# Kernel optimization log

Measured on AMD Instinct MI355X. Metric: run time of the kernel, lower is better.

## Reference

```python
import jax, jax.numpy as jnp
import numpy as np

B, Tin, Tout = 256, 32, 29
Venc, Vdec = 29, 72
E = 256; H = 256; L = 3; G = 4 * H; D = 2 * L  # bidirectional dirs * layers


def lstm_step(x, h, c, Wih0, Wih1, Whh, b):
    """One timestep of a 3-layer bidirectional LSTM (torch gate order i,f,g,o).
    x: [B, in], h/c: [D, B, H] in torch layout (layer-major, dir-minor)."""
    new_h, new_c = [], []
    inp = x
    for l in range(L):
        outs = []
        for d in range(2):
            idx = 2 * l + d
            Wih = Wih0[d] if l == 0 else Wih1[l - 1, d]
            g = inp @ Wih.T + h[idx] @ Whh[l, d].T + b[l, d]
            i_g, f_g, g_g, o_g = jnp.split(g, 4, axis=-1)
            cc = jax.nn.sigmoid(f_g) * c[idx] + jax.nn.sigmoid(i_g) * jnp.tanh(g_g)
            hh = jax.nn.sigmoid(o_g) * jnp.tanh(cc)
            new_h.append(hh); new_c.append(cc); outs.append(hh)
        inp = jnp.concatenate(outs, axis=-1)  # feeds next layer: [B, 2H]
    return jnp.stack(new_h), jnp.stack(new_c), inp


def proj(hid, W1, b1, W2, b2):
    """Linear over hidden dim then Linear over the layer*dir dim -- the exact
    math of torch's linear1 -> permute(2,1,0) -> linear2 -> permute(2,1,0)."""
    hn = jnp.einsum('lbh,gh->lbg', hid, W1) + b1            # [D, B, H]
    return jnp.einsum('lbh,ml->mbh', hn, W2) + b2[:, None, None]


def setup_inputs() -> dict:
    key = jax.random.key(0)
    ks = iter(jax.random.split(key, 64))
    def p(shape, scale=0.06):
        return jax.random.normal(next(ks), shape, jnp.float32) * scale
    return {
        "input": jax.random.randint(next(ks), (B, Tin), 0, Venc),
        "target": jax.random.randint(next(ks), (B, Tout), 0, Vdec),
        "teacher_force": 1,
        "enc_emb": p((Venc, E)), "dec_emb": p((Vdec, E)),
        "enc_Wih0": p((2, G, E)), "enc_Wih1": p((L - 1, 2, G, 2 * H)),
        "enc_Whh": p((L, 2, G, H)), "enc_b": p((L, 2, G)),
        "dec_Wih0": p((2, G, E)), "dec_Wih1": p((L - 1, 2, G, 2 * H)),
        "dec_Whh": p((L, 2, G, H)), "dec_b": p((L, 2, G)),
        "lin_h_W1": p((H, H)), "lin_h_b1": p((H,)), "lin_h_W2": p((D, D)), "lin_h_b2": p((D,)),
        "lin_c_W1": p((H, H)), "lin_c_b1": p((H,)), "lin_c_W2": p((D, D)), "lin_c_b2": p((D,)),
        "lin_a_W1": p((H, H)), "lin_a_b1": p((H,)), "lin_a_W2": p((D, D)), "lin_a_b2": p((D,)),
        "attn_W": p((E, E + H)), "attn_b": p((E,)),
        "fc_W": p((Vdec, 2 * H)), "fc_b": p((Vdec,)),
    }


def reference(input, target, teacher_force, enc_emb, dec_emb, enc_Wih0, enc_Wih1, enc_Whh, enc_b, dec_Wih0, dec_Wih1, dec_Whh, dec_b, lin_h_W1, lin_h_b1, lin_h_W2, lin_h_b2, lin_c_W1, lin_c_b1, lin_c_W2, lin_c_b2, lin_a_W1, lin_a_b1, lin_a_W2, lin_a_b2, attn_W, attn_b, fc_W, fc_b):
    Bb = input.shape[0]
    h0 = jnp.zeros((D, Bb, H), jnp.float32)

    # ---- encoder: step LSTM over Tin, projecting hidden per step for attention ----
    def enc_step(carry, x_t):
        h, c = carry
        h, c, _ = lstm_step(enc_emb[x_t], h, c, enc_Wih0, enc_Wih1, enc_Whh, enc_b)
        return (h, c), proj(h, lin_a_W1, lin_a_b1, lin_a_W2, lin_a_b2)

    (h, c), encoder_outputs = jax.lax.scan(enc_step, (h0, h0), input.T)  # [Tin, D, B, H]

    # ---- encoder->decoder state bridging (linear over H, linear over D) ----
    dec_h = proj(h, lin_h_W1, lin_h_b1, lin_h_W2, lin_h_b2)
    dec_c = proj(c, lin_c_W1, lin_c_b1, lin_c_W2, lin_c_b2)

    def dec_core(h, c, tok):
        emb = dec_emb[tok]                                # [B, E]
        energies = h[None] * encoder_outputs              # [Tin, D, B, H]
        aw = jax.nn.softmax(energies, axis=0)             # attn over source time
        ctx = (aw * encoder_outputs).sum(0).mean(0)       # [B, H]
        x = jnp.concatenate([emb, ctx], -1) @ attn_W.T + attn_b
        h, c, top = lstm_step(x, h, c, dec_Wih0, dec_Wih1, dec_Whh, dec_b)
        return h, c, top @ fc_W.T + fc_b, aw.sum(-1)      # logits [B,V], aw [Tin,D,B]

    if teacher_force:
        def step(carry, tok):
            h, c = carry
            h, c, logits, _ = dec_core(h, c, tok)
            return (h, c), logits
        _, logits_seq = jax.lax.scan(step, (dec_h, dec_c), target[:, :Tout - 1].T)
        attn_seq = jnp.zeros((Tout - 1, Tin, D, Bb), jnp.float32)
    else:
        def step(carry, _):
            h, c, tok = carry
            h, c, logits, aw = dec_core(h, c, tok)
            nxt = jnp.argmax(jax.nn.softmax(logits, -1), -1).astype(tok.dtype)
            return (h, c, nxt), (logits, aw)
        tok0 = jnp.ones((Bb,), input.dtype)
        _, (logits_seq, attn_seq) = jax.lax.scan(step, (dec_h, dec_c, tok0), None, length=Tout - 1)

    pred0 = jnp.zeros((1, Bb, Vdec), jnp.float32).at[0, :, 1].set(1.0)
    predicted = jnp.concatenate([pred0, logits_seq], 0)   # [Tout, B, Vdec]
    attn_weights = jnp.concatenate([jnp.zeros((1, Tin, D, Bb), jnp.float32), attn_seq], 0)
    return predicted, attn_weights
```

## Files before the change

### kernel.cpp

```cpp
#include <hip/hip_runtime.h>
#include <math.h>

#define BB 256
#define TIN 32
#define TOUT 29
#define VDEC 72
#define EDIM 256
#define HDIM 256
#define DD 6
#define BH (BB*HDIM)

typedef unsigned short u16;
typedef unsigned int u32;
typedef __bf16 bf16x8 __attribute__((ext_vector_type(8)));
typedef float f32x4 __attribute__((ext_vector_type(4)));
typedef u16 u16x8 __attribute__((ext_vector_type(8)));

__device__ __forceinline__ float sigmf(float x){ return 1.0f/(1.0f+expf(-x)); }
__device__ __forceinline__ u16 f2bf(float f){
  u32 u = __builtin_bit_cast(u32, f);
  u32 r = (u + 0x7fffu + ((u>>16)&1u)) >> 16;
  return (u16)r;
}
__device__ __forceinline__ float bf2f(u16 s){
  u32 u = ((u32)s)<<16; return __builtin_bit_cast(float, u);
}
__device__ __forceinline__ bf16x8 ldbf8(const u16* p){
  u16x8 t = *(const u16x8*)p; return __builtin_bit_cast(bf16x8, t);
}
__device__ __forceinline__ f32x4 mfma16(bf16x8 a, bf16x8 b, f32x4 c){
  return __builtin_amdgcn_mfma_f32_16x16x32_bf16(a, b, c, 0, 0, 0);
}

__global__ void fill_zero_u32(u32* __restrict__ p, int n){
  int i = blockIdx.x*256 + threadIdx.x;
  if (i < n) p[i] = 0u;
}

__global__ void init_out_kernel(float* __restrict__ out, int n){
  int i = blockIdx.x*256 + threadIdx.x;
  if (i >= n) return;
  float v = 0.0f;
  if (i < BB*VDEC && (i % VDEC) == 1) v = 1.0f;
  out[i] = v;
}

__global__ void bias2d_kernel(const float* __restrict__ W2a, const float* __restrict__ b1a, const float* __restrict__ b2a,
                              const float* __restrict__ W2h, const float* __restrict__ b1h, const float* __restrict__ b2h,
                              const float* __restrict__ W2c, const float* __restrict__ b1c, const float* __restrict__ b2c,
                              float* __restrict__ outp){
  int g = threadIdx.x;
  const float* W2[3] = {W2a, W2h, W2c};
  const float* b1[3] = {b1a, b1h, b1c};
  const float* b2[3] = {b2a, b2h, b2c};
  for (int p = 0; p < 3; p++)
    for (int m = 0; m < 6; m++){
      float s = 0.f;
      for (int l = 0; l < 6; l++) s += W2[p][m*6+l];
      outp[p*1536 + m*256 + g] = s * b1[p][g] + b2[p][m];
    }
}

__global__ void embed_enc_kernel(const int* __restrict__ input, const float* __restrict__ enc_emb,
                                 u16* __restrict__ x_emb){
  int i = blockIdx.x*256 + threadIdx.x;
  int e = i & 255, b = (i >> 8) & 255, t = i >> 16;
  x_emb[i] = f2bf(enc_emb[(size_t)input[b*TIN + t]*EDIM + e]);
}

__global__ void pack_w_kernel(const float* __restrict__ Wih, const float* __restrict__ Whh,
                              u16* __restrict__ dst, int K1, int K, int permute){
  int k = blockIdx.x*256 + threadIdx.x;
  int row = blockIdx.y;
  int d = row >> 10, rr = row & 1023;
  int g;
  if (permute){
    int ht = rr >> 6, r = rr & 63;
    g = (r>>4)*256 + ht*16 + (r&15);
  } else g = rr;
  float v;
  if (k < K1) v = Wih[((size_t)d*1024 + g)*K1 + k];
  else        v = Whh[((size_t)d*1024 + g)*256 + (k - K1)];
  dst[(size_t)row*K + k] = f2bf(v);
}

__global__ void mix_kernel(const float* __restrict__ inp, float* __restrict__ outp,
                           const float* __restrict__ W2, int n){
  int i = blockIdx.x*256 + threadIdx.x;
  if (i >= n) return;
  int h = i & 255, b = (i >> 8) & 255, t = i >> 16;
  size_t base = ((size_t)t*6)*BH + (size_t)b*256 + h;
  float v[6];
  #pragma unroll
  for (int l = 0; l < 6; l++) v[l] = inp[base + (size_t)l*BH];
  #pragma unroll
  for (int m = 0; m < 6; m++){
    float s = 0.f;
    #pragma unroll
    for (int l = 0; l < 6; l++) s += W2[m*6+l]*v[l];
    outp[base + (size_t)m*BH] = s;
  }
}

__global__ __launch_bounds__(256) void gemmN256_kernel(const float* __restrict__ A, float* __restrict__ C,
                                                       const float* __restrict__ W,
                                                       const float* __restrict__ bias2d,
                                                       u16* __restrict__ Cbf){
  __shared__ float As[32][33];
  __shared__ float Ws[256][34];
  int tid = threadIdx.x;
  int m_base = blockIdx.x * 32;
  int rg = tid >> 5, cg = tid & 31;
  float acc[4][8];
  #pragma unroll
  for (int i=0;i<4;i++)
    #pragma unroll
    for (int j=0;j<8;j++) acc[i][j]=0.f;
  for (int k0 = 0; k0 < 256; k0 += 32){
    #pragma unroll
    for (int p=0;p<4;p++) As[rg + p*8][cg] = A[(size_t)(m_base + rg + p*8)*256 + k0 + cg];
    #pragma unroll
    for (int p=0;p<32;p++) Ws[rg + p*8][cg] = W[(size_t)(rg + p*8)*256 + k0 + cg];
    __syncthreads();
    #pragma unroll
    for (int kk=0; kk<32; kk++){
      float a[4], w[8];
      #pragma unroll
      for (int i=0;i<4;i++) a[i] = As[rg*4+i][kk];
      #pragma unroll
      for (int j=0;j<8;j++) w[j] = Ws[cg*8+j][kk];
      #pragma unroll
      for (int i=0;i<4;i++)
        #pragma unroll
        for (int j=0;j<8;j++) acc[i][j] += a[i]*w[j];
    }
    __syncthreads();
  }
  #pragma unroll
  for (int i=0;i<4;i++){
    int row = m_base + rg*4 + i;
    int bm = (row >> 8) % 6;
    #pragma unroll
    for (int j=0;j<8;j++){
      float v = acc[i][j] + bias2d[bm*256 + cg*8 + j];
      C[(size_t)row*256 + cg*8 + j] = v;
      if (Cbf) Cbf[(size_t)row*256 + cg*8 + j] = f2bf(v);
    }
  }
}

__global__ __launch_bounds__(256) void lstm_stage_mfma(
    const u16* __restrict__ inp, int lda, int K1,
    const u16* __restrict__ Wpk,
    const float* __restrict__ bias_l,
    const u16* __restrict__ hR, u16* __restrict__ hW,
    float* __restrict__ cBuf, u16* __restrict__ inp_out,
    float* __restrict__ h_all_t, int l){
  __shared__ __align__(16) u16 As[32][72];
  __shared__ __align__(16) u16 Ws[64][72];
  __shared__ float Gt[4][32][17];
  int tid = threadIdx.x;
  int m_base = blockIdx.x*32;
  int d = blockIdx.y >> 4, ht = blockIdx.y & 15;
  int idx = 2*l + d;
  int K = K1 + 256;
  const u16* Wblk = Wpk + (size_t)((d*16+ht)*64)*K;
  const u16* A2 = hR + (size_t)idx*BH;
  int q = tid >> 6, lane = tid & 63;
  int ar = tid >> 3, kp = (tid & 7)*8;
  f32x4 acc0 = {0.f,0.f,0.f,0.f}, acc1 = {0.f,0.f,0.f,0.f};
  for (int c0 = 0; c0 < K; c0 += 64){
    int col = c0 + kp;
    const u16* ap = (col < K1) ? inp + (size_t)(m_base+ar)*lda + col
                               : A2  + (size_t)(m_base+ar)*HDIM + (col - K1);
    uint4 av  = *(const uint4*)ap;
    uint4 wv0 = *(const uint4*)(Wblk + (size_t)ar*K + col);
    uint4 wv1 = *(const uint4*)(Wblk + (size_t)(ar+32)*K + col);
    __syncthreads();
    *(uint4*)&As[ar][kp] = av;
    *(uint4*)&Ws[ar][kp] = wv0;
    *(uint4*)&Ws[ar+32][kp] = wv1;
    __syncthreads();
    #pragma unroll
    for (int kh = 0; kh < 2; kh++){
      int kb = kh*32 + (lane>>4)*8;
      bf16x8 a0 = ldbf8(&As[lane & 15][kb]);
      bf16x8 a1 = ldbf8(&As[16 + (lane & 15)][kb]);
      bf16x8 bq = ldbf8(&Ws[q*16 + (lane & 15)][kb]);
      acc0 = mfma16(a0, bq, acc0);
      acc1 = mfma16(a1, bq, acc1);
    }
  }
  int hh = lane & 15, rq = lane >> 4;
  #pragma unroll
  for (int r = 0; r < 4; r++){
    Gt[q][rq*4 + r][hh]      = acc0[r];
    Gt[q][16 + rq*4 + r][hh] = acc1[r];
  }
  __syncthreads();
  const float* bias = bias_l + d*1024;
  #pragma unroll
  for (int it = 0; it < 2; it++){
    int id = tid + it*256;
    int bb = id >> 4, h2 = id & 15;
    int b = m_base + bb, h = ht*16 + h2;
    float iv = Gt[0][bb][h2] + bias[h];
    float fv = Gt[1][bb][h2] + bias[256 + h];
    float gv = Gt[2][bb][h2] + bias[512 + h];
    float ov = Gt[3][bb][h2] + bias[768 + h];
    size_t off = (size_t)idx*BH + (size_t)b*HDIM + h;
    float cold = cBuf[off];
    float cc = sigmf(fv)*cold + sigmf(iv)*tanhf(gv);
    float hv = sigmf(ov)*tanhf(cc);
    cBuf[off] = cc;
    u16 hb = f2bf(hv);
    hW[off] = hb;
    inp_out[(size_t)b*512 + d*HDIM + h] = hb;
    if (h_all_t) h_all_t[off] = hv;
  }
}

__global__ __launch_bounds__(256) void xw_mfma(
    const u16* __restrict__ emb, const u16* __restrict__ ctx,
    const u16* __restrict__ Wpk, const float* __restrict__ bias,
    u16* __restrict__ xw){
  __shared__ __align__(16) u16 As[32][72];
  __shared__ __align__(16) u16 Ws[64][72];
  int tid = threadIdx.x;
  int m_base = blockIdx.x*32;
  int n_base = blockIdx.y*64;
  int q = tid >> 6, lane = tid & 63;
  int ar = tid >> 3, kp = (tid & 7)*8;
  const u16* Wblk = Wpk + (size_t)n_base*512;
  f32x4 acc0 = {0.f,0.f,0.f,0.f}, acc1 = {0.f,0.f,0.f,0.f};
  for (int c0 = 0; c0 < 512; c0 += 64){
    int col = c0 + kp;
    const u16* ap = (col < 256) ? emb + (size_t)(m_base+ar)*256 + col
                                : ctx + (size_t)(m_base+ar)*256 + (col - 256);
    uint4 av  = *(const uint4*)ap;
    uint4 wv0 = *(const uint4*)(Wblk + (size_t)ar*512 + col);
    uint4 wv1 = *(const uint4*)(Wblk + (size_t)(ar+32)*512 + col);
    __syncthreads();
    *(uint4*)&As[ar][kp] = av;
    *(uint4*)&Ws[ar][kp] = wv0;
    *(uint4*)&Ws[ar+32][kp] = wv1;
    __syncthreads();
    #pragma unroll
    for (int kh = 0; kh < 2; kh++){
      int kb = kh*32 + (lane>>4)*8;
      bf16x8 a0 = ldbf8(&As[lane & 15][kb]);
      bf16x8 a1 = ldbf8(&As[16 + (lane & 15)][kb]);
      bf16x8 bq = ldbf8(&Ws[q*16 + (lane & 15)][kb]);
      acc0 = mfma16(a0, bq, acc0);
      acc1 = mfma16(a1, bq, acc1);
    }
  }
  int hh = lane & 15, rq = lane >> 4;
  int n = n_base + q*16 + hh;
  float bv = bias[n];
  #pragma unroll
  for (int r = 0; r < 4; r++){
    xw[(size_t)(m_base + rq*4 + r)*256 + n]      = f2bf(acc0[r] + bv);
    xw[(size_t)(m_base + 16 + rq*4 + r)*256 + n] = f2bf(acc1[r] + bv);
  }
}

__global__ void attn_tok_kernel(const u16* __restrict__ hR, const float* __restrict__ eo,
                                u16* __restrict__ ctx, const int* __restrict__ tf,
                                float* __restrict__ attn_out, int step,
                                const int* __restrict__ target, const float* __restrict__ pred,
                                const float* __restrict__ dec_emb, u16* __restrict__ emb){
  int blk = blockIdx.x, tid = threadIdx.x;
  if (blk < 256){
    int i = blk*256 + tid;
    int hc = i & 255, b = i >> 8;
    bool wa = (tf[0] == 0);
    float acc = 0.f;
    for (int d = 0; d < DD; d++){
      float hv = bf2f(hR[(size_t)d*BH + (size_t)b*256 + hc]);
      const float* ep = eo + (size_t)d*BH + (size_t)b*256 + hc;
      float se = 0.f, ac = 0.f;
      for (int t = 0; t < TIN; t++){
        float ev = ep[(size_t)t*(DD*BH)];
        float e = expf(hv*ev);
        se += e; ac += e*ev;
      }
      acc += ac/se;
      if (wa){
        float inv = 1.f/se;
        for (int t = 0; t < TIN; t++){
          float ev = ep[(size_t)t*(DD*BH)];
          atomicAdd(&attn_out[(((size_t)(step+1)*TIN + t)*DD + d)*BB + b], expf(hv*ev)*inv);
        }
      }
    }
    ctx[i] = f2bf(acc*(1.0f/6.0f));
  } else {
    int j = (blk - 256)*256 + tid;
    int b = j >> 6, e4 = (j & 63)*4;
    int tok;
    if (tf[0]) tok = target[b*TOUT + step];
    else if (step == 0) tok = 1;
    else {
      const float* lg = pred + ((size_t)step*BB + b)*VDEC;
      tok = 0; float bv = lg[0];
      for (int v = 1; v < VDEC; v++){ float x = lg[v]; if (x > bv){ bv = x; tok = v; } }
    }
    #pragma unroll
    for (int r = 0; r < 4; r++)
      emb[(size_t)b*EDIM + e4 + r] = f2bf(dec_emb[(size_t)tok*EDIM + e4 + r]);
  }
}

__global__ void fc_kernel(const u16* __restrict__ top, const float* __restrict__ fc_W,
                          const float* __restrict__ fc_b, float* __restrict__ outp, int step){
  __shared__ float s[512];
  int b = blockIdx.x, tid = threadIdx.x;
  s[tid]       = bf2f(top[(size_t)b*512 + tid]);
  s[tid + 256] = bf2f(top[(size_t)b*512 + 256 + tid]);
  __syncthreads();
  if (tid < VDEC){
    float a = fc_b[tid];
    for (int k = 0; k < 512; k++) a += s[k]*fc_W[(size_t)tid*512 + k];
    outp[((size_t)(step+1)*BB + b)*VDEC + tid] = a;
  }
}


extern "C" void kernel_launch(void* const* d_in, const int* in_sizes, int n_in,
                              void* d_out, int out_size, void* d_ws, size_t ws_size,
                              hipStream_t stream){
  (void)in_sizes; (void)n_in; (void)out_size; (void)ws_size;
  const int*   input    = (const int*)d_in[0];
  const int*   target   = (const int*)d_in[1];
  const int*   tf       = (const int*)d_in[2];
  const float* enc_emb  = (const float*)d_in[3];
  const float* dec_emb  = (const float*)d_in[4];
  const float* enc_Wih0 = (const float*)d_in[5];
  const float* enc_Wih1 = (const float*)d_in[6];
  const float* enc_Whh  = (const float*)d_in[7];
  const float* enc_b    = (const float*)d_in[8];
  const float* dec_Wih0 = (const float*)d_in[9];
  const float* dec_Wih1 = (const float*)d_in[10];
  const float* dec_Whh  = (const float*)d_in[11];
  const float* dec_b    = (const float*)d_in[12];
  const float* lin_h_W1 = (const float*)d_in[13];
  const float* lin_h_b1 = (const float*)d_in[14];
  const float* lin_h_W2 = (const float*)d_in[15];
  const float* lin_h_b2 = (const float*)d_in[16];
  const float* lin_c_W1 = (const float*)d_in[17];
  const float* lin_c_b1 = (const float*)d_in[18];
  const float* lin_c_W2 = (const float*)d_in[19];
  const float* lin_c_b2 = (const float*)d_in[20];
  const float* lin_a_W1 = (const float*)d_in[21];
  const float* lin_a_b1 = (const float*)d_in[22];
  const float* lin_a_W2 = (const float*)d_in[23];
  const float* lin_a_b2 = (const float*)d_in[24];
  const float* attn_W   = (const float*)d_in[25];
  const float* attn_b   = (const float*)d_in[26];
  const float* fc_W     = (const float*)d_in[27];
  const float* fc_b     = (const float*)d_in[28];
  float* out = (float*)d_out;

  char* base = (char*)d_ws;
  size_t off = 0;
  auto alloc = [&](size_t bytes)->char*{
    char* p = base + off; off += (bytes + 255) & ~(size_t)255; return p;
  };
  float* h_all  = (float*)alloc(sizeof(float)*(size_t)TIN*DD*BH);
  float* tmp6   = (float*)alloc(sizeof(float)*(size_t)DD*BH);
  float* dec_c  = (float*)alloc(sizeof(float)*(size_t)DD*BH);
  float* bias2d = (float*)alloc(sizeof(float)*3*6*256);
  u16*   enc_hA = (u16*)alloc(sizeof(u16)*(size_t)DD*BH + sizeof(float)*(size_t)DD*BH);
  float* enc_c  = (float*)(enc_hA + (size_t)DD*BH);
  u16* enc_hB = (u16*)alloc(sizeof(u16)*(size_t)DD*BH);
  u16* dec_hA = (u16*)alloc(sizeof(u16)*(size_t)DD*BH);
  u16* dec_hB = (u16*)alloc(sizeof(u16)*(size_t)DD*BH);
  u16* x_emb  = (u16*)alloc(sizeof(u16)*(size_t)TIN*BB*EDIM);
  u16* bufA   = (u16*)alloc(sizeof(u16)*(size_t)BB*512);
  u16* bufB   = (u16*)alloc(sizeof(u16)*(size_t)BB*512);
  u16* emb    = (u16*)alloc(sizeof(u16)*(size_t)BB*256);
  u16* ctxb   = (u16*)alloc(sizeof(u16)*(size_t)BB*256);
  u16* xw     = (u16*)alloc(sizeof(u16)*(size_t)BB*256);
  u16* wp_e0  = (u16*)alloc(sizeof(u16)*(size_t)2048*512);
  u16* wp_e1  = (u16*)alloc(sizeof(u16)*(size_t)2048*768);
  u16* wp_e2  = (u16*)alloc(sizeof(u16)*(size_t)2048*768);
  u16* wp_d0  = (u16*)alloc(sizeof(u16)*(size_t)2048*512);
  u16* wp_d1  = (u16*)alloc(sizeof(u16)*(size_t)2048*768);
  u16* wp_d2  = (u16*)alloc(sizeof(u16)*(size_t)2048*768);
  u16* wp_at  = (u16*)alloc(sizeof(u16)*(size_t)256*512);

  const int outn = TOUT*BB*VDEC + TOUT*TIN*DD*BB;
  init_out_kernel<<<(outn+255)/256, 256, 0, stream>>>(out, outn);
  fill_zero_u32<<<(DD*BH*6/4 + 255)/256, 256, 0, stream>>>((u32*)enc_hA, DD*BH*6/4);
  bias2d_kernel<<<1, 256, 0, stream>>>(lin_a_W2, lin_a_b1, lin_a_b2,
                                       lin_h_W2, lin_h_b1, lin_h_b2,
                                       lin_c_W2, lin_c_b1, lin_c_b2, bias2d);
  embed_enc_kernel<<<(TIN*BB*EDIM)/256, 256, 0, stream>>>(input, enc_emb, x_emb);
  pack_w_kernel<<<dim3(2,2048), 256, 0, stream>>>(enc_Wih0, enc_Whh,                       wp_e0, 256, 512, 1);
  pack_w_kernel<<<dim3(3,2048), 256, 0, stream>>>(enc_Wih1, enc_Whh + 2*1024*256,          wp_e1, 512, 768, 1);
  pack_w_kernel<<<dim3(3,2048), 256, 0, stream>>>(enc_Wih1 + (size_t)2*1024*512, enc_Whh + 4*1024*256, wp_e2, 512, 768, 1);
  pack_w_kernel<<<dim3(2,2048), 256, 0, stream>>>(dec_Wih0, dec_Whh,                       wp_d0, 256, 512, 1);
  pack_w_kernel<<<dim3(3,2048), 256, 0, stream>>>(dec_Wih1, dec_Whh + 2*1024*256,          wp_d1, 512, 768, 1);
  pack_w_kernel<<<dim3(3,2048), 256, 0, stream>>>(dec_Wih1 + (size_t)2*1024*512, dec_Whh + 4*1024*256, wp_d2, 512, 768, 1);
  pack_w_kernel<<<dim3(2,256),  256, 0, stream>>>(attn_W, attn_W ,               wp_at, 512, 512, 0);

  dim3 sgrid(8, 32);
  for (int t = 0; t < TIN; t++){
    const u16* hRb = (t & 1) ? enc_hB : enc_hA;
    u16*       hWb = (t & 1) ? enc_hA : enc_hB;
    float* hat = h_all + (size_t)t*DD*BH;
    lstm_stage_mfma<<<sgrid,256,0,stream>>>(x_emb + (size_t)t*BB*EDIM, 256, 256, wp_e0,
        enc_b,        hRb, hWb, enc_c, bufA, hat, 0);
    lstm_stage_mfma<<<sgrid,256,0,stream>>>(bufA, 512, 512, wp_e1,
        enc_b + 2048, hRb, hWb, enc_c, bufB, hat, 1);
    lstm_stage_mfma<<<sgrid,256,0,stream>>>(bufB, 512, 512, wp_e2,
        enc_b + 4096, hRb, hWb, enc_c, bufA, hat, 2);
  }
  mix_kernel<<<BH/256, 256, 0, stream>>>(h_all + (size_t)31*DD*BH, tmp6, lin_h_W2, BH);
  gemmN256_kernel<<<(DD*BB)/32, 256, 0, stream>>>(tmp6, tmp6, lin_h_W1, bias2d + 1536, dec_hA);
  mix_kernel<<<BH/256, 256, 0, stream>>>(enc_c, tmp6, lin_c_W2, BH);
  gemmN256_kernel<<<(DD*BB)/32, 256, 0, stream>>>(tmp6, dec_c, lin_c_W1, bias2d + 3072, nullptr);
  mix_kernel<<<(TIN*BH)/256, 256, 0, stream>>>(h_all, h_all, lin_a_W2, TIN*BH);
  gemmN256_kernel<<<(TIN*DD*BB)/32, 256, 0, stream>>>(h_all, h_all, lin_a_W1, bias2d, nullptr);

  float* attn_out = out + (size_t)TOUT*BB*VDEC;
  for (int i = 0; i < TOUT-1; i++){
    const u16* hRb = (i & 1) ? dec_hB : dec_hA;
    u16*       hWb = (i & 1) ? dec_hA : dec_hB;
    attn_tok_kernel<<<320, 256, 0, stream>>>(hRb, h_all, ctxb, tf, attn_out, i,
                                             target, out, dec_emb, emb);
    xw_mfma<<<dim3(8,4), 256, 0, stream>>>(emb, ctxb, wp_at, attn_b, xw);
    lstm_stage_mfma<<<sgrid,256,0,stream>>>(xw, 256, 256, wp_d0,
        dec_b,        hRb, hWb, dec_c, bufA, nullptr, 0);
    lstm_stage_mfma<<<sgrid,256,0,stream>>>(bufA, 512, 512, wp_d1,
        dec_b + 2048, hRb, hWb, dec_c, bufB, nullptr, 1);
    lstm_stage_mfma<<<sgrid,256,0,stream>>>(bufB, 512, 512, wp_d2,
        dec_b + 4096, hRb, hWb, dec_c, bufA, nullptr, 2);
    fc_kernel<<<BB, 256, 0, stream>>>(bufA, fc_W, fc_b, out, i);
  }
}
```

Baseline: 3.429 ms.

## Fold attention linear into decoder weights, fuse fc into attention, double-buffer LSTM loads

Precomputes Wih0·attn_W and the matching bias so the decoder's attention-combine GEMM disappears and layer 0 reads the concatenated [emb, ctx] directly. The fc projection and argmax move into the attention/token kernel for the next step, which drops one launch per decoder step. Encoder outputs are now stored in bf16, halving attention read traffic. The LSTM stage kernel is templated on K, uses double-buffered register and shared-memory prefetch with a single barrier per iteration, and switches to fast exp/tanh. This trades accuracy (bf16 encoder outputs, folded weights rounded to bf16, approximate transcendentals) for fewer launches and less memory traffic.

```diff
diff --git a/kernel.cpp b/kernel.cpp
--- a/kernel.cpp
+++ b/kernel.cpp
@@ -16,7 +16,8 @@
 typedef float f32x4 __attribute__((ext_vector_type(4)));
 typedef u16 u16x8 __attribute__((ext_vector_type(8)));
 
-__device__ __forceinline__ float sigmf(float x){ return 1.0f/(1.0f+expf(-x)); }
+__device__ __forceinline__ float sigmf(float x){ return 1.0f/(1.0f+__expf(-x)); }
+__device__ __forceinline__ float tanhf_fast(float x){ return 1.0f - 2.0f/(1.0f+__expf(2.0f*x)); }
 __device__ __forceinline__ u16 f2bf(float f){
   u32 u = __builtin_bit_cast(u32, f);
   u32 r = (u + 0x7fffu + ((u>>16)&1u)) >> 16;
@@ -69,19 +70,46 @@
 }
 
 __global__ void pack_w_kernel(const float* __restrict__ Wih, const float* __restrict__ Whh,
-                              u16* __restrict__ dst, int K1, int K, int permute){
+                              u16* __restrict__ dst, int K1, int K){
   int k = blockIdx.x*256 + threadIdx.x;
   int row = blockIdx.y;
   int d = row >> 10, rr = row & 1023;
-  int g;
-  if (permute){
-    int ht = rr >> 6, r = rr & 63;
-    g = (r>>4)*256 + ht*16 + (r&15);
-  } else g = rr;
+  int ht = rr >> 6, r = rr & 63;
+  int g = (r>>4)*256 + ht*16 + (r&15);
   float v;
   if (k < K1) v = Wih[((size_t)d*1024 + g)*K1 + k];
   else        v = Whh[((size_t)d*1024 + g)*256 + (k - K1)];
   dst[(size_t)row*K + k] = f2bf(v);
+}
+
+__global__ void pack_wfused_kernel(const float* __restrict__ Wih0, const float* __restrict__ attn_W,
+                                   const float* __restrict__ Whh, u16* __restrict__ dst){
+  int k = blockIdx.x*256 + threadIdx.x;
+  int row = blockIdx.y;
+  int d = row >> 10, rr = row & 1023;
+  int ht = rr >> 6, r = rr & 63;
+  int g = (r>>4)*256 + ht*16 + (r&15);
+  float v;
+  if (k >= 512) v = Whh[((size_t)d*1024 + g)*256 + (k - 512)];
+  else {
+    const float* wr = Wih0 + ((size_t)d*1024 + g)*256;
+    float s = 0.f;
+    #pragma unroll 4
+    for (int o = 0; o < 256; o++) s += wr[o] * attn_W[(size_t)o*512 + k];
+    v = s;
+  }
+  dst[(size_t)row*768 + k] = f2bf(v);
+}
+
+__global__ void biasfold_kernel(const float* __restrict__ Wih0, const float* __restrict__ attn_b,
+                                const float* __restrict__ dec_b, float* __restrict__ outb){
+  int i = blockIdx.x*256 + threadIdx.x;
+  int d = i >> 10, g = i & 1023;
+  const float* wr = Wih0 + ((size_t)d*1024 + g)*256;
+  float s = dec_b[d*1024 + g];
+  #pragma unroll 4
+  for (int o = 0; o < 256; o++) s += wr[o]*attn_b[o];
+  outb[i] = s;
 }
 
 __global__ void mix_kernel(const float* __restrict__ inp, float* __restrict__ outp,
@@ -143,50 +171,66 @@
     #pragma unroll
     for (int j=0;j<8;j++){
       float v = acc[i][j] + bias2d[bm*256 + cg*8 + j];
-      C[(size_t)row*256 + cg*8 + j] = v;
+      if (C)   C[(size_t)row*256 + cg*8 + j] = v;
       if (Cbf) Cbf[(size_t)row*256 + cg*8 + j] = f2bf(v);
     }
   }
 }
 
+template<int K1>
 __global__ __launch_bounds__(256) void lstm_stage_mfma(
-    const u16* __restrict__ inp, int lda, int K1,
+    const u16* __restrict__ inp,
     const u16* __restrict__ Wpk,
     const float* __restrict__ bias_l,
     const u16* __restrict__ hR, u16* __restrict__ hW,
     float* __restrict__ cBuf, u16* __restrict__ inp_out,
     float* __restrict__ h_all_t, int l){
-  __shared__ __align__(16) u16 As[32][72];
-  __shared__ __align__(16) u16 Ws[64][72];
+  constexpr int K = K1 + 256;
+  constexpr int NIT = K >> 6;
+  __shared__ __align__(16) u16 As[2][32][72];
+  __shared__ __align__(16) u16 Ws[2][64][72];
   __shared__ float Gt[4][32][17];
   int tid = threadIdx.x;
   int m_base = blockIdx.x*32;
   int d = blockIdx.y >> 4, ht = blockIdx.y & 15;
   int idx = 2*l + d;
-  int K = K1 + 256;
   const u16* Wblk = Wpk + (size_t)((d*16+ht)*64)*K;
-  const u16* A2 = hR + (size_t)idx*BH;
   int q = tid >> 6, lane = tid & 63;
   int ar = tid >> 3, kp = (tid & 7)*8;
+  const u16* aRow  = inp + (size_t)(m_base+ar)*K1 + kp;
+  const u16* hRow  = hR + (size_t)idx*BH + (size_t)(m_base+ar)*HDIM + kp - K1;
+  const u16* wRow0 = Wblk + (size_t)ar*K + kp;
+  const u16* wRow1 = Wblk + (size_t)(ar+32)*K + kp;
+  uint4 aP[2], w0P[2], w1P[2];
+  #pragma unroll
+  for (int pf = 0; pf < 2; pf++){
+    int c0 = pf*64;
+    const u16* ap = (c0 + kp < K1) ? aRow : hRow;
+    aP[pf]  = *(const uint4*)(ap + c0);
+    w0P[pf] = *(const uint4*)(wRow0 + c0);
+    w1P[pf] = *(const uint4*)(wRow1 + c0);
+  }
   f32x4 acc0 = {0.f,0.f,0.f,0.f}, acc1 = {0.f,0.f,0.f,0.f};
-  for (int c0 = 0; c0 < K; c0 += 64){
-    int col = c0 + kp;
-    const u16* ap = (col < K1) ? inp + (size_t)(m_base+ar)*lda + col
-                               : A2  + (size_t)(m_base+ar)*HDIM + (col - K1);
-    uint4 av  = *(const uint4*)ap;
-    uint4 wv0 = *(const uint4*)(Wblk + (size_t)ar*K + col);
-    uint4 wv1 = *(const uint4*)(Wblk + (size_t)(ar+32)*K + col);
-    __syncthreads();
-    *(uint4*)&As[ar][kp] = av;
-    *(uint4*)&Ws[ar][kp] = wv0;
-    *(uint4*)&Ws[ar+32][kp] = wv1;
+  #pragma unroll
+  for (int i = 0; i < NIT; i++){
+    int p = i & 1;
+    *(uint4*)&As[p][ar][kp]     = aP[p];
+    *(uint4*)&Ws[p][ar][kp]     = w0P[p];
+    *(uint4*)&Ws[p][ar+32][kp]  = w1P[p];
+    int c0n = (i+2) << 6;
+    if (c0n < K){
+      const u16* ap = (c0n + kp < K1) ? aRow : hRow;
+      aP[p]  = *(const uint4*)(ap + c0n);
+      w0P[p] = *(const uint4*)(wRow0 + c0n);
+      w1P[p] = *(const uint4*)(wRow1 + c0n);
+    }
     __syncthreads();
     #pragma unroll
     for (int kh = 0; kh < 2; kh++){
       int kb = kh*32 + (lane>>4)*8;
-      bf16x8 a0 = ldbf8(&As[lane & 15][kb]);
-      bf16x8 a1 = ldbf8(&As[16 + (lane & 15)][kb]);
-      bf16x8 bq = ldbf8(&Ws[q*16 + (lane & 15)][kb]);
+      bf16x8 a0 = ldbf8(&As[p][lane & 15][kb]);
+      bf16x8 a1 = ldbf8(&As[p][16 + (lane & 15)][kb]);
+      bf16x8 bq = ldbf8(&Ws[p][q*16 + (lane & 15)][kb]);
       acc0 = mfma16(a0, bq, acc0);
       acc1 = mfma16(a1, bq, acc1);
     }
@@ -210,8 +254,8 @@
     float ov = Gt[3][bb][h2] + bias[768 + h];
     size_t off = (size_t)idx*BH + (size_t)b*HDIM + h;
     float cold = cBuf[off];
-    float cc = sigmf(fv)*cold + sigmf(iv)*tanhf(gv);
-    float hv = sigmf(ov)*tanhf(cc);
+    float cc = sigmf(fv)*cold + sigmf(iv)*tanhf_fast(gv);
+    float hv = sigmf(ov)*tanhf_fast(cc);
     cBuf[off] = cc;
     u16 hb = f2bf(hv);
     hW[off] = hb;
@@ -220,95 +264,68 @@
   }
 }
 
-__global__ __launch_bounds__(256) void xw_mfma(
-    const u16* __restrict__ emb, const u16* __restrict__ ctx,
-    const u16* __restrict__ Wpk, const float* __restrict__ bias,
-    u16* __restrict__ xw){
-  __shared__ __align__(16) u16 As[32][72];
-  __shared__ __align__(16) u16 Ws[64][72];
-  int tid = threadIdx.x;
-  int m_base = blockIdx.x*32;
-  int n_base = blockIdx.y*64;
-  int q = tid >> 6, lane = tid & 63;
-  int ar = tid >> 3, kp = (tid & 7)*8;
-  const u16* Wblk = Wpk + (size_t)n_base*512;
-  f32x4 acc0 = {0.f,0.f,0.f,0.f}, acc1 = {0.f,0.f,0.f,0.f};
-  for (int c0 = 0; c0 < 512; c0 += 64){
-    int col = c0 + kp;
-    const u16* ap = (col < 256) ? emb + (size_t)(m_base+ar)*256 + col
-                                : ctx + (size_t)(m_base+ar)*256 + (col - 256);
-    uint4 av  = *(const uint4*)ap;
-    uint4 wv0 = *(const uint4*)(Wblk + (size_t)ar*512 + col);
-    uint4 wv1 = *(const uint4*)(Wblk + (size_t)(ar+32)*512 + col);
-    __syncthreads();
-    *(uint4*)&As[ar][kp] = av;
-    *(uint4*)&Ws[ar][kp] = wv0;
-    *(uint4*)&Ws[ar+32][kp] = wv1;
-    __syncthreads();
-    #pragma unroll
-    for (int kh = 0; kh < 2; kh++){
-      int kb = kh*32 + (lane>>4)*8;
-      bf16x8 a0 = ldbf8(&As[lane & 15][kb]);
-      bf16x8 a1 = ldbf8(&As[16 + (lane & 15)][kb]);
-      bf16x8 bq = ldbf8(&Ws[q*16 + (lane & 15)][kb]);
-      acc0 = mfma16(a0, bq, acc0);
-      acc1 = mfma16(a1, bq, acc1);
-    }
-  }
-  int hh = lane & 15, rq = lane >> 4;
-  int n = n_base + q*16 + hh;
-  float bv = bias[n];
-  #pragma unroll
-  for (int r = 0; r < 4; r++){
-    xw[(size_t)(m_base + rq*4 + r)*256 + n]      = f2bf(acc0[r] + bv);
-    xw[(size_t)(m_base + 16 + rq*4 + r)*256 + n] = f2bf(acc1[r] + bv);
-  }
-}
-
-__global__ void attn_tok_kernel(const u16* __restrict__ hR, const float* __restrict__ eo,
-                                u16* __restrict__ ctx, const int* __restrict__ tf,
+__global__ void attn_tok_kernel(const u16* __restrict__ hR, const u16* __restrict__ eo,
+                                u16* __restrict__ cat, const int* __restrict__ tf,
                                 float* __restrict__ attn_out, int step,
-                                const int* __restrict__ target, const float* __restrict__ pred,
-                                const float* __restrict__ dec_emb, u16* __restrict__ emb){
+                                const int* __restrict__ target, float* __restrict__ outp,
+                                const float* __restrict__ dec_emb, const u16* __restrict__ top,
+                                const float* __restrict__ fc_W, const float* __restrict__ fc_b){
   int blk = blockIdx.x, tid = threadIdx.x;
+  __shared__ float s[512];
+  __shared__ float lg[VDEC];
+  __shared__ int tokS;
   if (blk < 256){
-    int i = blk*256 + tid;
-    int hc = i & 255, b = i >> 8;
+    int b = blk, hc = tid;
     bool wa = (tf[0] == 0);
     float acc = 0.f;
     for (int d = 0; d < DD; d++){
       float hv = bf2f(hR[(size_t)d*BH + (size_t)b*256 + hc]);
-      const float* ep = eo + (size_t)d*BH + (size_t)b*256 + hc;
+      const u16* ep = eo + (size_t)d*BH + (size_t)b*256 + hc;
       float se = 0.f, ac = 0.f;
+      #pragma unroll 8
       for (int t = 0; t < TIN; t++){
-        float ev = ep[(size_t)t*(DD*BH)];
-        float e = expf(hv*ev);
+        float ev = bf2f(ep[(size_t)t*(DD*BH)]);
+        float e = __expf(hv*ev);
         se += e; ac += e*ev;
       }
       acc += ac/se;
       if (wa){
         float inv = 1.f/se;
         for (int t = 0; t < TIN; t++){
-          float ev = ep[(size_t)t*(DD*BH)];
-          atomicAdd(&attn_out[(((size_t)(step+1)*TIN + t)*DD + d)*BB + b], expf(hv*ev)*inv);
+          float ev = bf2f(ep[(size_t)t*(DD*BH)]);
+          atomicAdd(&attn_out[(((size_t)(step+1)*TIN + t)*DD + d)*BB + b], __expf(hv*ev)*inv);
         }
       }
     }
-    ctx[i] = f2bf(acc*(1.0f/6.0f));
+    cat[(size_t)b*512 + 256 + hc] = f2bf(acc*(1.0f/6.0f));
   } else {
-    int j = (blk - 256)*256 + tid;
-    int b = j >> 6, e4 = (j & 63)*4;
+    int b = blk - 256;
+    if (step > 0){
+      s[tid]       = bf2f(top[(size_t)b*512 + tid]);
+      s[tid + 256] = bf2f(top[(size_t)b*512 + 256 + tid]);
+      __syncthreads();
+      if (tid < VDEC){
+        float a = fc_b[tid];
+        #pragma unroll 4
+        for (int k = 0; k < 512; k++) a += s[k]*fc_W[(size_t)tid*512 + k];
+        outp[((size_t)step*BB + b)*VDEC + tid] = a;
+        lg[tid] = a;
+      }
+      __syncthreads();
+    }
     int tok;
     if (tf[0]) tok = target[b*TOUT + step];
     else if (step == 0) tok = 1;
     else {
-      const float* lg = pred + ((size_t)step*BB + b)*VDEC;
-      tok = 0; float bv = lg[0];
-      for (int v = 1; v < VDEC; v++){ float x = lg[v]; if (x > bv){ bv = x; tok = v; } }
-    }
-    #pragma unroll
-    for (int r = 0; r < 4; r++)
-      emb[(size_t)b*EDIM + e4 + r] = f2bf(dec_emb[(size_t)tok*EDIM + e4 + r]);
+      if (tid == 0){
+        int bi = 0; float bv = lg[0];
+        for (int v = 1; v < VDEC; v++){ float x = lg[v]; if (x > bv){ bv = x; bi = v; } }
+        tokS = bi;
+      }
+      __syncthreads();
+      tok = tokS;
+    }
+    cat[(size_t)b*512 + tid] = f2bf(dec_emb[(size_t)tok*EDIM + tid]);
   }
 }
 
@@ -321,6 +338,7 @@
   __syncthreads();
   if (tid < VDEC){
     float a = fc_b[tid];
+    #pragma unroll 4
     for (int k = 0; k < 512; k++) a += s[k]*fc_W[(size_t)tid*512 + k];
     outp[((size_t)(step+1)*BB + b)*VDEC + tid] = a;
   }
@@ -379,16 +397,15 @@
   u16* x_emb  = (u16*)alloc(sizeof(u16)*(size_t)TIN*BB*EDIM);
   u16* bufA   = (u16*)alloc(sizeof(u16)*(size_t)BB*512);
   u16* bufB   = (u16*)alloc(sizeof(u16)*(size_t)BB*512);
-  u16* emb    = (u16*)alloc(sizeof(u16)*(size_t)BB*256);
-  u16* ctxb   = (u16*)alloc(sizeof(u16)*(size_t)BB*256);
-  u16* xw     = (u16*)alloc(sizeof(u16)*(size_t)BB*256);
+  u16* cat    = (u16*)alloc(sizeof(u16)*(size_t)BB*512);
+  u16* eo_bf  = (u16*)alloc(sizeof(u16)*(size_t)TIN*DD*BH);
   u16* wp_e0  = (u16*)alloc(sizeof(u16)*(size_t)2048*512);
   u16* wp_e1  = (u16*)alloc(sizeof(u16)*(size_t)2048*768);
   u16* wp_e2  = (u16*)alloc(sizeof(u16)*(size_t)2048*768);
-  u16* wp_d0  = (u16*)alloc(sizeof(u16)*(size_t)2048*512);
+  u16* wp_d0f = (u16*)alloc(sizeof(u16)*(size_t)2048*768);
   u16* wp_d1  = (u16*)alloc(sizeof(u16)*(size_t)2048*768);
   u16* wp_d2  = (u16*)alloc(sizeof(u16)*(size_t)2048*768);
-  u16* wp_at  = (u16*)alloc(sizeof(u16)*(size_t)256*512);
+  float* fb0  = (float*)alloc(sizeof(float)*2048);
 
   const int outn = TOUT*BB*VDEC + TOUT*TIN*DD*BB;
   init_out_kernel<<<(outn+255)/256, 256, 0, stream>>>(out, outn);
@@ -397,46 +414,45 @@
                                        lin_h_W2, lin_h_b1, lin_h_b2,
                                        lin_c_W2, lin_c_b1, lin_c_b2, bias2d);
   embed_enc_kernel<<<(TIN*BB*EDIM)/256, 256, 0, stream>>>(input, enc_emb, x_emb);
-  pack_w_kernel<<<dim3(2,2048), 256, 0, stream>>>(enc_Wih0, enc_Whh,                       wp_e0, 256, 512, 1);
-  pack_w_kernel<<<dim3(3,2048), 256, 0, stream>>>(enc_Wih1, enc_Whh + 2*1024*256,          wp_e1, 512, 768, 1);
-  pack_w_kernel<<<dim3(3,2048), 256, 0, stream>>>(enc_Wih1 + (size_t)2*1024*512, enc_Whh + 4*1024*256, wp_e2, 512, 768, 1);
-  pack_w_kernel<<<dim3(2,2048), 256, 0, stream>>>(dec_Wih0, dec_Whh,                       wp_d0, 256, 512, 1);
-  pack_w_kernel<<<dim3(3,2048), 256, 0, stream>>>(dec_Wih1, dec_Whh + 2*1024*256,          wp_d1, 512, 768, 1);
-  pack_w_kernel<<<dim3(3,2048), 256, 0, stream>>>(dec_Wih1 + (size_t)2*1024*512, dec_Whh + 4*1024*256, wp_d2, 512, 768, 1);
-  pack_w_kernel<<<dim3(2,256),  256, 0, stream>>>(attn_W, attn_W ,               wp_at, 512, 512, 0);
+  pack_w_kernel<<<dim3(2,2048), 256, 0, stream>>>(enc_Wih0, enc_Whh,                       wp_e0, 256, 512);
+  pack_w_kernel<<<dim3(3,2048), 256, 0, stream>>>(enc_Wih1, enc_Whh + 2*1024*256,          wp_e1, 512, 768);
+  pack_w_kernel<<<dim3(3,2048), 256, 0, stream>>>(enc_Wih1 + (size_t)2*1024*512, enc_Whh + 4*1024*256, wp_e2, 512, 768);
+  pack_wfused_kernel<<<dim3(3,2048), 256, 0, stream>>>(dec_Wih0, attn_W, dec_Whh,          wp_d0f);
+  biasfold_kernel<<<8, 256, 0, stream>>>(dec_Wih0, attn_b, dec_b, fb0);
+  pack_w_kernel<<<dim3(3,2048), 256, 0, stream>>>(dec_Wih1, dec_Whh + 2*1024*256,          wp_d1, 512, 768);
+  pack_w_kernel<<<dim3(3,2048), 256, 0, stream>>>(dec_Wih1 + (size_t)2*1024*512, dec_Whh + 4*1024*256, wp_d2, 512, 768);
 
   dim3 sgrid(8, 32);
   for (int t = 0; t < TIN; t++){
     const u16* hRb = (t & 1) ? enc_hB : enc_hA;
     u16*       hWb = (t & 1) ? enc_hA : enc_hB;
     float* hat = h_all + (size_t)t*DD*BH;
-    lstm_stage_mfma<<<sgrid,256,0,stream>>>(x_emb + (size_t)t*BB*EDIM, 256, 256, wp_e0,
+    lstm_stage_mfma<256><<<sgrid,256,0,stream>>>(x_emb + (size_t)t*BB*EDIM, wp_e0,
         enc_b,        hRb, hWb, enc_c, bufA, hat, 0);
-    lstm_stage_mfma<<<sgrid,256,0,stream>>>(bufA, 512, 512, wp_e1,
+    lstm_stage_mfma<512><<<sgrid,256,0,stream>>>(bufA, wp_e1,
         enc_b + 2048, hRb, hWb, enc_c, bufB, hat, 1);
-    lstm_stage_mfma<<<sgrid,256,0,stream>>>(bufB, 512, 512, wp_e2,
+    lstm_stage_mfma<512><<<sgrid,256,0,stream>>>(bufB, wp_e2,
         enc_b + 4096, hRb, hWb, enc_c, bufA, hat, 2);
   }
   mix_kernel<<<BH/256, 256, 0, stream>>>(h_all + (size_t)31*DD*BH, tmp6, lin_h_W2, BH);
-  gemmN256_kernel<<<(DD*BB)/32, 256, 0, stream>>>(tmp6, tmp6, lin_h_W1, bias2d + 1536, dec_hA);
+  gemmN256_kernel<<<(DD*BB)/32, 256, 0, stream>>>(tmp6, nullptr, lin_h_W1, bias2d + 1536, dec_hA);
   mix_kernel<<<BH/256, 256, 0, stream>>>(enc_c, tmp6, lin_c_W2, BH);
   gemmN256_kernel<<<(DD*BB)/32, 256, 0, stream>>>(tmp6, dec_c, lin_c_W1, bias2d + 3072, nullptr);
   mix_kernel<<<(TIN*BH)/256, 256, 0, stream>>>(h_all, h_all, lin_a_W2, TIN*BH);
-  gemmN256_kernel<<<(TIN*DD*BB)/32, 256, 0, stream>>>(h_all, h_all, lin_a_W1, bias2d, nullptr);
+  gemmN256_kernel<<<(TIN*DD*BB)/32, 256, 0, stream>>>(h_all, nullptr, lin_a_W1, bias2d, eo_bf);
 
   float* attn_out = out + (size_t)TOUT*BB*VDEC;
   for (int i = 0; i < TOUT-1; i++){
     const u16* hRb = (i & 1) ? dec_hB : dec_hA;
     u16*       hWb = (i & 1) ? dec_hA : dec_hB;
-    attn_tok_kernel<<<320, 256, 0, stream>>>(hRb, h_all, ctxb, tf, attn_out, i,
-                                             target, out, dec_emb, emb);
-    xw_mfma<<<dim3(8,4), 256, 0, stream>>>(emb, ctxb, wp_at, attn_b, xw);
-    lstm_stage_mfma<<<sgrid,256,0,stream>>>(xw, 256, 256, wp_d0,
-        dec_b,        hRb, hWb, dec_c, bufA, nullptr, 0);
-    lstm_stage_mfma<<<sgrid,256,0,stream>>>(bufA, 512, 512, wp_d1,
+    attn_tok_kernel<<<512, 256, 0, stream>>>(hRb, eo_bf, cat, tf, attn_out, i,
+                                             target, out, dec_emb, bufA, fc_W, fc_b);
+    lstm_stage_mfma<512><<<sgrid,256,0,stream>>>(cat,  wp_d0f,
+        fb0,          hRb, hWb, dec_c, bufA, nullptr, 0);
+    lstm_stage_mfma<512><<<sgrid,256,0,stream>>>(bufA, wp_d1,
         dec_b + 2048, hRb, hWb, dec_c, bufB, nullptr, 1);
-    lstm_stage_mfma<<<sgrid,256,0,stream>>>(bufB, 512, 512, wp_d2,
+    lstm_stage_mfma<512><<<sgrid,256,0,stream>>>(bufB, wp_d2,
         dec_b + 4096, hRb, hWb, dec_c, bufA, nullptr, 2);
-    fc_kernel<<<BB, 256, 0, stream>>>(bufA, fc_W, fc_b, out, i);
-  }
-}
+  }
+  fc_kernel<<<BB, 256, 0, stream>>>(bufA, fc_W, fc_b, out, TOUT-2);
+}
```

Measured after the change: 3.751 ms. 1.09x slower.
